# Kernel optimization log

Measured on AMD Instinct MI355X. Metric: run time of the kernel, lower is better.

The kernel has to match this reference:

```python
import jax, jax.numpy as jnp
import numpy as np

VAR0, VAR1 = 0.1, 0.2
POS_TH, NEG_TH = 0.5, 0.5
NEG_POS_RATIO = 10

def point_form(c):
    # center-size (cx,cy,w,h) -> corners (x1,y1,x2,y2)
    return jnp.concatenate([c[..., :2] - c[..., 2:] / 2, c[..., :2] + c[..., 2:] / 2], axis=-1)

def iou(a, b):
    # corner-form boxes, broadcastable [..., 4]
    lt = jnp.maximum(a[..., :2], b[..., :2])
    rb = jnp.minimum(a[..., 2:], b[..., 2:])
    wh = jnp.clip(rb - lt, 0.0)
    inter = wh[..., 0] * wh[..., 1]
    area_a = (a[..., 2] - a[..., 0]) * (a[..., 3] - a[..., 1])
    area_b = (b[..., 2] - b[..., 0]) * (b[..., 3] - b[..., 1])
    return inter / (area_a + area_b - inter)

def encode(matched, priors):
    # matched: corner-form gt boxes; priors: center-size anchors
    g_cxcy = ((matched[..., :2] + matched[..., 2:]) * 0.5 - priors[..., :2]) / (VAR0 * priors[..., 2:])
    g_wh = jnp.log((matched[..., 2:] - matched[..., :2]) / priors[..., 2:]) / VAR1
    return jnp.concatenate([g_cxcy, g_wh], axis=-1)

def smooth_l1(d):
    ad = jnp.abs(d)
    return jnp.where(ad < 1.0, 0.5 * ad * ad, ad - 0.5)

def setup_inputs() -> dict:
    key = jax.random.key(0)
    ks = jax.random.split(key, 8)
    B, O, A = 8, 32, 16384
    cxy = jax.random.uniform(ks[0], (A, 2), minval=0.1, maxval=0.9)
    wh = jax.random.uniform(ks[1], (A, 2), minval=0.05, maxval=0.3)
    anchors = jnp.concatenate([cxy, wh], axis=-1)  # [A,4] center-size
    # ground-truth boxes jittered around random anchors so matching finds positives
    idx = jax.random.randint(ks[2], (B, O), 0, A)
    base = point_form(anchors)[idx]  # [B,O,4] corner form
    boxes = base + jax.random.uniform(ks[3], (B, O, 4), minval=-0.01, maxval=0.01)
    counts = jax.random.randint(ks[4], (B,), 4, O)  # valid objects per image
    pad = jnp.arange(O)[None, :] >= counts[:, None]
    cls = jax.random.randint(ks[5], (B, O), 0, 2)
    true_classes = jnp.where(pad, -1, cls).astype(jnp.int32)
    true_boxes = jnp.where(pad[..., None], -1.0, boxes)
    pred_boxes = 0.5 * jax.random.normal(ks[6], (B, A, 4))
    pred_classes = jax.random.normal(ks[7], (B, A, 2))
    return dict(pred_boxes=pred_boxes, pred_classes=pred_classes,
                true_boxes=true_boxes, true_classes=true_classes, anchors=anchors)

def detection_loss(pred_boxes, pred_classes, true_boxes, true_classes, anchors):
    dtype = pred_boxes.dtype
    pad = true_classes < 0  # [B,O]
    # --- anchor matching (IoU between corner-form anchors and gt boxes) ---
    overlap = iou(point_form(anchors)[None, None, :, :], true_boxes[:, :, None, :])  # [B,O,A]
    overlap = jnp.where(pad[..., None], -1.0, overlap)
    best = overlap.max(axis=1, keepdims=True)  # best gt per anchor
    positive = (jnp.abs(best - overlap) < 1e-6) & (overlap > POS_TH)  # [B,O,A]
    negative = overlap.max(axis=1) < NEG_TH  # [B,A]
    n_pos = positive.sum()
    denom = jnp.maximum(n_pos, 1).astype(dtype)
    # --- box loss: SmoothL1(sum) on encoded positives only ---
    dummy = jnp.array([0.3, 0.3, 0.5, 0.5], dtype)  # valid dummy box for padded slots (masked out)
    tb = jnp.where(pad[..., None], dummy, true_boxes)
    enc = encode(tb[:, :, None, :], anchors[None, None, :, :])  # [B,O,A,4]
    d = jnp.where(positive[..., None], pred_boxes[:, None, :, :] - enc, 0.0)
    box_loss = 1.0 * smooth_l1(d).sum() / denom
    # --- class loss: positives + hard-negative mining, weighted CE mean ---
    logp = jax.nn.log_softmax(pred_classes, axis=-1)  # [B,A,2]
    cls = jnp.clip(true_classes, 0, 1)
    ce_pos = -jnp.where((cls == 1)[:, :, None], logp[:, None, :, 1], logp[:, None, :, 0])  # [B,O,A]
    w = jnp.where(cls == 1, 4.0, 1.0)[:, :, None]
    sum_pos = jnp.sum(positive * w * ce_pos)
    wsum_pos = jnp.sum(positive * w)
    # negatives: target class 0 (weight 1); mining rank == CE value
    neg_ce = jnp.where(negative, -logp[..., 0], -jnp.inf).reshape(-1)  # [B*A]
    sorted_desc = jnp.sort(neg_ce)[::-1]
    n_neg = negative.sum()
    k = jnp.minimum(NEG_POS_RATIO * n_pos, n_neg)
    take = jnp.arange(sorted_desc.shape[0]) < k
    sum_neg = jnp.sum(jnp.where(take, sorted_desc, 0.0))
    cls_loss = 10.0 * (sum_pos + sum_neg) / jnp.maximum(wsum_pos + k.astype(dtype), 1e-6) / denom
    total = box_loss + cls_loss
    return box_loss, cls_loss, total

def reference(pred_boxes, pred_classes, true_boxes, true_classes, anchors):
    return detection_loss(pred_boxes, pred_classes, true_boxes, true_classes, anchors)
```

## Files before the change

### kernel.cpp

```cpp
#include <hip/hip_runtime.h>
#include <math.h>

#define NOBJ  32
#define NANCH 16384
#define NTOT  131072
#define MBLK  256
#define NREP  8
#define NBUK  2048
#define BOFF  1792

#define OFF_SLOTS 64
#define OFF_HC    2112
#define HWORDS    (NREP * NBUK * 2)

__device__ __forceinline__ float smooth_l1f(float d) {
    float ad = fabsf(d);
    return ad < 1.0f ? 0.5f * ad * ad : ad - 0.5f;
}

__global__ __launch_bounds__(256) void dl_zero(unsigned int* __restrict__ ws)
{
    int i = blockIdx.x * 256 + threadIdx.x;
    reinterpret_cast<uint4*>(ws + OFF_HC)[i] = make_uint4(0u, 0u, 0u, 0u);
}

__global__ __launch_bounds__(512) void dl_main(
    const float* __restrict__ pred_boxes,
    const float* __restrict__ pred_classes,
    const float* __restrict__ true_boxes,
    const int*   __restrict__ true_classes,
    const float* __restrict__ anchors,
    unsigned int* __restrict__ ws)
{
    __shared__ float    s_tb[NOBJ * 4];
    __shared__ int      s_tc[NOBJ];
    __shared__ unsigned lcnt[2][NBUK];
    __shared__ float    lsum[2][NBUK];
    __shared__ int      s_wi[8][2];
    __shared__ float    s_wf[8][3];

    const int t = threadIdx.x;
    const int idx = blockIdx.x * 512 + t;
    const int b = idx >> 14;
    const int a = idx & (NANCH - 1);
    if (t < NOBJ * 4) s_tb[t] = true_boxes[b * NOBJ * 4 + t];
    if (t < NOBJ)     s_tc[t] = true_classes[b * NOBJ + t];
    for (int i = t; i < 2 * NBUK; i += 512) { (&lcnt[0][0])[i] = 0u; (&lsum[0][0])[i] = 0.f; }
    __syncthreads();

    float4 anc = reinterpret_cast<const float4*>(anchors)[a];
    float ax1 = anc.x - anc.z * 0.5f;
    float ay1 = anc.y - anc.w * 0.5f;
    float ax2 = anc.x + anc.z * 0.5f;
    float ay2 = anc.y + anc.w * 0.5f;
    float area_a = (ax2 - ax1) * (ay2 - ay1);

    float ov[NOBJ];
    float best = -3.402823466e38f;
#pragma unroll
    for (int o = 0; o < NOBJ; ++o) {
        float v;
        if (s_tc[o] < 0) {
            v = -1.0f;
        } else {
            float bx1 = s_tb[o * 4 + 0], by1 = s_tb[o * 4 + 1];
            float bx2 = s_tb[o * 4 + 2], by2 = s_tb[o * 4 + 3];
            float ltx = fmaxf(ax1, bx1), lty = fmaxf(ay1, by1);
            float rbx = fminf(ax2, bx2), rby = fminf(ay2, by2);
            float w = fmaxf(rbx - ltx, 0.0f), h = fmaxf(rby - lty, 0.0f);
            float inter = w * h;
            float area_b = (bx2 - bx1) * (by2 - by1);
            v = inter / (area_a + area_b - inter);
        }
        ov[o] = v;
        best = fmaxf(best, v);
    }

    float2 pc = reinterpret_cast<const float2*>(pred_classes)[idx];
    float mx = fmaxf(pc.x, pc.y);
    float lse = mx + logf(expf(pc.x - mx) + expf(pc.y - mx));
    float l0 = pc.x - lse;
    float l1 = pc.y - lse;

    const int wave = t >> 6, lane = t & 63, rep = wave & 1;
    int isneg = 0;
    if (best < 0.5f) {
        float nce = -l0;
        int bk = (int)(__float_as_uint(nce) >> 19) - BOFF;
        bk = bk < 0 ? 0 : (bk > NBUK - 1 ? NBUK - 1 : bk);
        atomicAdd(&lcnt[rep][bk], 1u);
        atomicAdd(&lsum[rep][bk], nce);
        isneg = 1;
    }

    float4 pb = reinterpret_cast<const float4*>(pred_boxes)[idx];
    int npos = 0; float boxs = 0.f, poss = 0.f, wsum = 0.f;
#pragma unroll
    for (int o = 0; o < NOBJ; ++o) {
        float v = ov[o];
        if (fabsf(best - v) < 1e-6f && v > 0.5f) {
            ++npos;
            float bx1 = s_tb[o * 4 + 0], by1 = s_tb[o * 4 + 1];
            float bx2 = s_tb[o * 4 + 2], by2 = s_tb[o * 4 + 3];
            float gcx = ((bx1 + bx2) * 0.5f - anc.x) / (0.1f * anc.z);
            float gcy = ((by1 + by2) * 0.5f - anc.y) / (0.1f * anc.w);
            float gw  = logf((bx2 - bx1) / anc.z) / 0.2f;
            float gh  = logf((by2 - by1) / anc.w) / 0.2f;
            boxs += smooth_l1f(pb.x - gcx) + smooth_l1f(pb.y - gcy)
                  + smooth_l1f(pb.z - gw)  + smooth_l1f(pb.w - gh);
            int c = s_tc[o];
            float w = (c == 1) ? 4.0f : 1.0f;
            poss += w * ((c == 1) ? -l1 : -l0);
            wsum += w;
        }
    }

    int ip = npos, ng = isneg;
    float fb = boxs, fp = poss, fw = wsum;
#pragma unroll
    for (int o = 32; o; o >>= 1) {
        ip += __shfl_down(ip, o); ng += __shfl_down(ng, o);
        fb += __shfl_down(fb, o); fp += __shfl_down(fp, o); fw += __shfl_down(fw, o);
    }
    if (lane == 0) {
        s_wi[wave][0] = ip; s_wi[wave][1] = ng;
        s_wf[wave][0] = fb; s_wf[wave][1] = fp; s_wf[wave][2] = fw;
    }
    __syncthreads();
    if (t == 0) {
        int tp = 0, tn = 0; float t2 = 0.f, t3 = 0.f, t4 = 0.f;
        for (int w = 0; w < 8; ++w) {
            tp += s_wi[w][0]; tn += s_wi[w][1];
            t2 += s_wf[w][0]; t3 += s_wf[w][1]; t4 += s_wf[w][2];
        }
        unsigned* sl = ws + OFF_SLOTS + blockIdx.x * 8;
        sl[0] = (unsigned)tp; sl[1] = (unsigned)tn;
        sl[2] = __float_as_uint(t2); sl[3] = __float_as_uint(t3); sl[4] = __float_as_uint(t4);
    }
    unsigned* gc = ws + OFF_HC + (blockIdx.x & (NREP - 1)) * (NBUK * 2);
    float*    gs = reinterpret_cast<float*>(gc + NBUK);
    for (int i = t; i < NBUK; i += 512) {
        unsigned c = lcnt[0][i] + lcnt[1][i];
        if (c) { atomicAdd(gc + i, c); atomicAdd(gs + i, lsum[0][i] + lsum[1][i]); }
    }
}

__global__ __launch_bounds__(1024) void dl_tail(const unsigned int* __restrict__ ws,
                                                float* __restrict__ out)
{
    __shared__ int   s_wi[16][2];
    __shared__ float s_wf[16][3];
    __shared__ int   wti[16];
    __shared__ float wtf[16];
    __shared__ int   sh_k;
    __shared__ float sh_fp, sh_fw, sh_box, sh_denom;

    const int t = threadIdx.x, wave = t >> 6, lane = t & 63;

    int np = 0, nn = 0; float fb = 0.f, fp = 0.f, fw = 0.f;
    if (t < MBLK) {
        const unsigned* sl = ws + OFF_SLOTS + t * 8;
        np = (int)sl[0]; nn = (int)sl[1];
        fb = __uint_as_float(sl[2]); fp = __uint_as_float(sl[3]); fw = __uint_as_float(sl[4]);
    }
#pragma unroll
    for (int o = 32; o; o >>= 1) {
        np += __shfl_down(np, o); nn += __shfl_down(nn, o);
        fb += __shfl_down(fb, o); fp += __shfl_down(fp, o); fw += __shfl_down(fw, o);
    }
    if (lane == 0 && wave < 4) {
        s_wi[wave][0] = np; s_wi[wave][1] = nn;
        s_wf[wave][0] = fb; s_wf[wave][1] = fp; s_wf[wave][2] = fw;
    }
    __syncthreads();
    if (t == 0) {
        int tp = 0, tn = 0; float t2 = 0.f, t3 = 0.f, t4 = 0.f;
        for (int w = 0; w < 4; ++w) {
            tp += s_wi[w][0]; tn += s_wi[w][1];
            t2 += s_wf[w][0]; t3 += s_wf[w][1]; t4 += s_wf[w][2];
        }
        long long k10 = 10LL * (long long)tp;
        int k = (int)((k10 < (long long)tn) ? k10 : (long long)tn);
        sh_k = k;
        sh_fp = t3; sh_fw = t4;
        sh_denom = (float)(tp > 1 ? tp : 1);
        sh_box = t2 / sh_denom;
    }
    __syncthreads();
    const int k = sh_k;
    if (k == 0) {
        if (t == 0) {
            float cls = 10.0f * sh_fp / fmaxf(sh_fw, 1e-6f) / sh_denom;
            out[0] = sh_box; out[1] = cls; out[2] = sh_box + cls;
        }
        return;
    }

    unsigned cbk[2] = {0u, 0u};
    float    sbk[2] = {0.f, 0.f};
#pragma unroll
    for (int r = 0; r < NREP; ++r) {
        uint2  u = *reinterpret_cast<const uint2*>(ws + OFF_HC + r * (NBUK * 2) + t * 2);
        float2 s = *reinterpret_cast<const float2*>(ws + OFF_HC + r * (NBUK * 2) + NBUK + t * 2);
        cbk[0] += u.x; cbk[1] += u.y;
        sbk[0] += s.x; sbk[1] += s.y;
    }
    int   cc = (int)(cbk[0] + cbk[1]);
    float ss = sbk[0] + sbk[1];

    int v = cc; float f = ss;
#pragma unroll
    for (int o = 1; o < 64; o <<= 1) {
        int   u2 = __shfl_down(v, o);
        float g2 = __shfl_down(f, o);
        if (lane + o < 64) { v += u2; f += g2; }
    }
    if (lane == 0) { wti[wave] = v; wtf[wave] = f; }
    __syncthreads();
    int S = v; float FS = f;
    for (int w = wave + 1; w < 16; ++w) { S += wti[w]; FS += wtf[w]; }

    if (S >= k && S - cc < k) {
        int   cum  = S - cc;
        float facc = FS - ss;
        float sfx = 0.f;
        for (int bq = 1; bq >= 0; --bq) {
            int cb = (int)cbk[bq];
            if (cum + cb >= k) {
                int r1 = k - cum;
                float sneg = facc + sfx + (float)r1 * (sbk[bq] / (float)cb);
                float cls = 10.0f * (sh_fp + sneg)
                          / fmaxf(sh_fw + (float)k, 1e-6f) / sh_denom;
                out[0] = sh_box; out[1] = cls; out[2] = sh_box + cls;
                break;
            }
            cum += cb; sfx += sbk[bq];
        }
    }
}

extern "C" void kernel_launch(void* const* d_in, const int* in_sizes, int n_in,
                              void* d_out, int out_size, void* d_ws, size_t ws_size,
                              hipStream_t stream)
{
    const float* pred_boxes   = (const float*)d_in[0];
    const float* pred_classes = (const float*)d_in[1];
    const float* true_boxes   = (const float*)d_in[2];
    const int*   true_classes = (const int*)d_in[3];
    const float* anchors      = (const float*)d_in[4];
    unsigned int* ws = (unsigned int*)d_ws;

    dl_zero<<<32, 256, 0, stream>>>(ws);
    dl_main<<<MBLK, 512, 0, stream>>>(pred_boxes, pred_classes, true_boxes,
                                      true_classes, anchors, ws);
    dl_tail<<<1, 1024, 0, stream>>>(ws, (float*)d_out);
}
```

Measured before the change: 26.21 us.

## Fuse tail reduction into main kernel via last-block-done atomic counter

```diff
diff --git a/kernel.cpp b/kernel.cpp
--- a/kernel.cpp
+++ b/kernel.cpp
@@ -10,18 +10,27 @@
 #define BOFF  1792
 
 #define OFF_SLOTS 64
-#define OFF_HC    2112
-#define HWORDS    (NREP * NBUK * 2)
+#define OFF_ARR   2112
+#define OFF_HC    2368
+#define ZERO_U4   8256
 
 __device__ __forceinline__ float smooth_l1f(float d) {
     float ad = fabsf(d);
     return ad < 1.0f ? 0.5f * ad * ad : ad - 0.5f;
 }
 
+__device__ __forceinline__ unsigned ld_au(const unsigned* p) {
+    return __hip_atomic_load(p, __ATOMIC_RELAXED, __HIP_MEMORY_SCOPE_AGENT);
+}
+__device__ __forceinline__ float ld_af(const float* p) {
+    return __hip_atomic_load(p, __ATOMIC_RELAXED, __HIP_MEMORY_SCOPE_AGENT);
+}
+
 __global__ __launch_bounds__(256) void dl_zero(unsigned int* __restrict__ ws)
 {
     int i = blockIdx.x * 256 + threadIdx.x;
-    reinterpret_cast<uint4*>(ws + OFF_HC)[i] = make_uint4(0u, 0u, 0u, 0u);
+    if (i < ZERO_U4)
+        reinterpret_cast<uint4*>(ws + OFF_ARR)[i] = make_uint4(0u, 0u, 0u, 0u);
 }
 
 __global__ __launch_bounds__(512) void dl_main(
@@ -30,7 +39,8 @@
     const float* __restrict__ true_boxes,
     const int*   __restrict__ true_classes,
     const float* __restrict__ anchors,
-    unsigned int* __restrict__ ws)
+    unsigned int* __restrict__ ws,
+    float* __restrict__ out)
 {
     __shared__ float    s_tb[NOBJ * 4];
     __shared__ int      s_tc[NOBJ];
@@ -38,6 +48,11 @@
     __shared__ float    lsum[2][NBUK];
     __shared__ int      s_wi[8][2];
     __shared__ float    s_wf[8][3];
+    __shared__ int      wti[8];
+    __shared__ float    wtf[8];
+    __shared__ int      s_fin;
+    __shared__ int      sh_k;
+    __shared__ float    sh_fp, sh_fw, sh_box, sh_denom;
 
     const int t = threadIdx.x;
     const int idx = blockIdx.x * 512 + t;
@@ -143,98 +158,108 @@
         unsigned c = lcnt[0][i] + lcnt[1][i];
         if (c) { atomicAdd(gc + i, c); atomicAdd(gs + i, lsum[0][i] + lsum[1][i]); }
     }
-}
-
-__global__ __launch_bounds__(1024) void dl_tail(const unsigned int* __restrict__ ws,
-                                                float* __restrict__ out)
-{
-    __shared__ int   s_wi[16][2];
-    __shared__ float s_wf[16][3];
-    __shared__ int   wti[16];
-    __shared__ float wtf[16];
-    __shared__ int   sh_k;
-    __shared__ float sh_fp, sh_fw, sh_box, sh_denom;
-
-    const int t = threadIdx.x, wave = t >> 6, lane = t & 63;
-
-    int np = 0, nn = 0; float fb = 0.f, fp = 0.f, fw = 0.f;
-    if (t < MBLK) {
-        const unsigned* sl = ws + OFF_SLOTS + t * 8;
-        np = (int)sl[0]; nn = (int)sl[1];
-        fb = __uint_as_float(sl[2]); fp = __uint_as_float(sl[3]); fw = __uint_as_float(sl[4]);
-    }
-#pragma unroll
-    for (int o = 32; o; o >>= 1) {
-        np += __shfl_down(np, o); nn += __shfl_down(nn, o);
-        fb += __shfl_down(fb, o); fp += __shfl_down(fp, o); fw += __shfl_down(fw, o);
-    }
-    if (lane == 0 && wave < 4) {
-        s_wi[wave][0] = np; s_wi[wave][1] = nn;
-        s_wf[wave][0] = fb; s_wf[wave][1] = fp; s_wf[wave][2] = fw;
-    }
+
+    __threadfence();
     __syncthreads();
     if (t == 0) {
-        int tp = 0, tn = 0; float t2 = 0.f, t3 = 0.f, t4 = 0.f;
-        for (int w = 0; w < 4; ++w) {
-            tp += s_wi[w][0]; tn += s_wi[w][1];
-            t2 += s_wf[w][0]; t3 += s_wf[w][1]; t4 += s_wf[w][2];
-        }
-        long long k10 = 10LL * (long long)tp;
-        int k = (int)((k10 < (long long)tn) ? k10 : (long long)tn);
-        sh_k = k;
-        sh_fp = t3; sh_fw = t4;
-        sh_denom = (float)(tp > 1 ? tp : 1);
-        sh_box = t2 / sh_denom;
-    }
-    __syncthreads();
-    const int k = sh_k;
-    if (k == 0) {
+        s_fin = 0;
+        int grp = blockIdx.x & (NREP - 1);
+        unsigned ga = __hip_atomic_fetch_add(ws + OFF_ARR + grp * 16, 1u,
+                                             __ATOMIC_ACQ_REL, __HIP_MEMORY_SCOPE_AGENT) + 1u;
+        if (ga == MBLK / NREP) {
+            unsigned ra = __hip_atomic_fetch_add(ws + OFF_ARR + 128, 1u,
+                                                 __ATOMIC_ACQ_REL, __HIP_MEMORY_SCOPE_AGENT) + 1u;
+            if (ra == NREP) s_fin = 1;
+        }
+    }
+    __syncthreads();
+    if (!s_fin) return;
+
+    {
+        int np = 0, nn = 0; float fb2 = 0.f, fp2 = 0.f, fw2 = 0.f;
+        if (t < MBLK) {
+            const unsigned* sl = ws + OFF_SLOTS + t * 8;
+            np = (int)ld_au(sl + 0); nn = (int)ld_au(sl + 1);
+            fb2 = ld_af((const float*)sl + 2);
+            fp2 = ld_af((const float*)sl + 3);
+            fw2 = ld_af((const float*)sl + 4);
+        }
+#pragma unroll
+        for (int o = 32; o; o >>= 1) {
+            np += __shfl_down(np, o); nn += __shfl_down(nn, o);
+            fb2 += __shfl_down(fb2, o); fp2 += __shfl_down(fp2, o); fw2 += __shfl_down(fw2, o);
+        }
+        if (lane == 0 && wave < 4) {
+            s_wi[wave][0] = np; s_wi[wave][1] = nn;
+            s_wf[wave][0] = fb2; s_wf[wave][1] = fp2; s_wf[wave][2] = fw2;
+        }
+        __syncthreads();
         if (t == 0) {
-            float cls = 10.0f * sh_fp / fmaxf(sh_fw, 1e-6f) / sh_denom;
-            out[0] = sh_box; out[1] = cls; out[2] = sh_box + cls;
-        }
-        return;
-    }
-
-    unsigned cbk[2] = {0u, 0u};
-    float    sbk[2] = {0.f, 0.f};
-#pragma unroll
-    for (int r = 0; r < NREP; ++r) {
-        uint2  u = *reinterpret_cast<const uint2*>(ws + OFF_HC + r * (NBUK * 2) + t * 2);
-        float2 s = *reinterpret_cast<const float2*>(ws + OFF_HC + r * (NBUK * 2) + NBUK + t * 2);
-        cbk[0] += u.x; cbk[1] += u.y;
-        sbk[0] += s.x; sbk[1] += s.y;
-    }
-    int   cc = (int)(cbk[0] + cbk[1]);
-    float ss = sbk[0] + sbk[1];
-
-    int v = cc; float f = ss;
-#pragma unroll
-    for (int o = 1; o < 64; o <<= 1) {
-        int   u2 = __shfl_down(v, o);
-        float g2 = __shfl_down(f, o);
-        if (lane + o < 64) { v += u2; f += g2; }
-    }
-    if (lane == 0) { wti[wave] = v; wtf[wave] = f; }
-    __syncthreads();
-    int S = v; float FS = f;
-    for (int w = wave + 1; w < 16; ++w) { S += wti[w]; FS += wtf[w]; }
-
-    if (S >= k && S - cc < k) {
-        int   cum  = S - cc;
-        float facc = FS - ss;
-        float sfx = 0.f;
-        for (int bq = 1; bq >= 0; --bq) {
-            int cb = (int)cbk[bq];
-            if (cum + cb >= k) {
-                int r1 = k - cum;
-                float sneg = facc + sfx + (float)r1 * (sbk[bq] / (float)cb);
-                float cls = 10.0f * (sh_fp + sneg)
-                          / fmaxf(sh_fw + (float)k, 1e-6f) / sh_denom;
+            int tp = 0, tn = 0; float t2 = 0.f, t3 = 0.f, t4 = 0.f;
+            for (int w = 0; w < 4; ++w) {
+                tp += s_wi[w][0]; tn += s_wi[w][1];
+                t2 += s_wf[w][0]; t3 += s_wf[w][1]; t4 += s_wf[w][2];
+            }
+            long long k10 = 10LL * (long long)tp;
+            int k = (int)((k10 < (long long)tn) ? k10 : (long long)tn);
+            sh_k = k;
+            sh_fp = t3; sh_fw = t4;
+            sh_denom = (float)(tp > 1 ? tp : 1);
+            sh_box = t2 / sh_denom;
+        }
+        __syncthreads();
+        const int k = sh_k;
+        if (k == 0) {
+            if (t == 0) {
+                float cls = 10.0f * sh_fp / fmaxf(sh_fw, 1e-6f) / sh_denom;
                 out[0] = sh_box; out[1] = cls; out[2] = sh_box + cls;
-                break;
-            }
-            cum += cb; sfx += sbk[bq];
+            }
+            return;
+        }
+
+        unsigned cbk[4] = {0u, 0u, 0u, 0u};
+        float    sbk[4] = {0.f, 0.f, 0.f, 0.f};
+#pragma unroll
+        for (int r = 0; r < NREP; ++r) {
+            const unsigned* gcr = ws + OFF_HC + r * (NBUK * 2);
+            const float*    gsr = (const float*)(gcr + NBUK);
+#pragma unroll
+            for (int i = 0; i < 4; ++i) {
+                cbk[i] += ld_au(gcr + t * 4 + i);
+                sbk[i] += ld_af(gsr + t * 4 + i);
+            }
+        }
+        int   cc = (int)(cbk[0] + cbk[1] + cbk[2] + cbk[3]);
+        float ss = sbk[0] + sbk[1] + sbk[2] + sbk[3];
+
+        int v = cc; float f = ss;
+#pragma unroll
+        for (int o = 1; o < 64; o <<= 1) {
+            int   u2 = __shfl_down(v, o);
+            float g2 = __shfl_down(f, o);
+            if (lane + o < 64) { v += u2; f += g2; }
+        }
+        if (lane == 0) { wti[wave] = v; wtf[wave] = f; }
+        __syncthreads();
+        int S = v; float FS = f;
+        for (int w = wave + 1; w < 8; ++w) { S += wti[w]; FS += wtf[w]; }
+
+        if (S >= k && S - cc < k) {
+            int   cum  = S - cc;
+            float facc = FS - ss;
+            float sfx = 0.f;
+            for (int bq = 3; bq >= 0; --bq) {
+                int cb = (int)cbk[bq];
+                if (cum + cb >= k) {
+                    int r1 = k - cum;
+                    float sneg = facc + sfx + (float)r1 * (sbk[bq] / (float)cb);
+                    float cls = 10.0f * (sh_fp + sneg)
+                              / fmaxf(sh_fw + (float)k, 1e-6f) / sh_denom;
+                    out[0] = sh_box; out[1] = cls; out[2] = sh_box + cls;
+                    break;
+                }
+                cum += cb; sfx += sbk[bq];
+            }
         }
     }
 }
@@ -250,8 +275,7 @@
     const float* anchors      = (const float*)d_in[4];
     unsigned int* ws = (unsigned int*)d_ws;
 
-    dl_zero<<<32, 256, 0, stream>>>(ws);
+    dl_zero<<<33, 256, 0, stream>>>(ws);
     dl_main<<<MBLK, 512, 0, stream>>>(pred_boxes, pred_classes, true_boxes,
-                                      true_classes, anchors, ws);
-    dl_tail<<<1, 1024, 0, stream>>>(ws, (float*)d_out);
-}
+                                      true_classes, anchors, ws, (float*)d_out);
+}
```

Measured after the change: 60.33 us. 2.3x slower.
